# Kernel optimization log

Hardware: AMD Instinct MI355X
Metric: run time of the kernel (lower is better)

The kernel has to match this reference:

```python
import jax, jax.numpy as jnp
import numpy as np

B, P, K, HE, HF = 256, 128, 512, 1024, 512
D = K + HE + 2 * HF  # 2560, MLP input dim
HID = 64


def setup_inputs() -> dict:
    key = jax.random.key(0)
    ks = jax.random.split(key, 6)
    query = jax.random.normal(ks[0], (B, 1, HE), dtype=jnp.float32)
    keys = jax.random.normal(ks[1], (B, P, K), dtype=jnp.float32)
    frameLSTM_h = jax.random.normal(ks[2], (B, 1, 2 * HF), dtype=jnp.float32)
    mask = jax.random.randint(ks[3], (B, P), 0, 2, dtype=jnp.int32)
    mask = mask.at[:, 0].set(1)  # guarantee at least one unmasked player per row
    W1 = jax.random.normal(ks[4], (D, HID), dtype=jnp.float32) / np.float32(np.sqrt(D))
    W2 = jax.random.normal(ks[5], (HID, 1), dtype=jnp.float32) / np.float32(np.sqrt(HID))
    return dict(query=query, keys=keys, frameLSTM_h=frameLSTM_h, mask=mask, W1=W1, W2=W2)


def reference(query, keys, frameLSTM_h, mask, W1, W2):
    # Faithful to: cat([keys, query.repeat, frame.repeat]) @ W1 -> ReLU -> @ W2.
    # The pre-activation is linear, so splitting W1 by row-blocks is exactly the
    # same math without materializing the repeated/concatenated (B,P,D) tensor.
    W1k = W1[:K]            # (K, 64)
    W1q = W1[K:K + HE]      # (HE, 64)
    W1f = W1[K + HE:]       # (2*HF, 64)
    h = jax.nn.relu(
        jnp.einsum('bpk,kh->bph', keys, W1k)
        + jnp.einsum('boe,eh->boh', query, W1q)        # broadcasts over P
        + jnp.einsum('bof,fh->boh', frameLSTM_h, W1f)  # broadcasts over P
    )  # (B, P, 64)
    raw_scores = jnp.einsum('bph,ho->bp', h, W2)  # (B, P)
    raw_scores = jnp.where(mask == 0, -jnp.inf, raw_scores)
    weights = jax.nn.softmax(raw_scores, axis=1)  # (B, P)
    context = jnp.einsum('bp,bpk->bk', weights, keys)[:, None, :]  # (B, 1, K)
    embeddings = jnp.concatenate([context, frameLSTM_h], axis=2)   # (B, 1, K+2*HF)
    return embeddings, weights
```

## Files before the change

### kernel.cpp

```cpp
#include <hip/hip_runtime.h>
#include <hip/hip_bf16.h>
#include <cstdint>
#include <math.h>


typedef __bf16 bf16;
typedef __attribute__((ext_vector_type(8))) __bf16 bf16x8;
typedef __attribute__((ext_vector_type(4))) __bf16 bf16x4;
typedef __attribute__((ext_vector_type(4))) float f32x4;

#define NB 256
#define NP 128
#define NK 512
#define SKLD 520
#define SK_BYTES (NP * SKLD * 2)
#define SMEM_BYTES (SK_BYTES + 128*4 + 128*4 + 256*4 + 64*4)

__global__ __launch_bounds__(256) void prep_kernel(
    const float* __restrict__ W1, bf16* __restrict__ w1kt,
    bf16* __restrict__ w1qft)
{
    const int blk = blockIdx.x;
    const int t = threadIdx.x;
    __shared__ float s[32][65];
    if (blk < 16) {
        const int k0 = blk * 32;
#pragma unroll
        for (int i = 0; i < 8; i++) {
            const int idx = t + 256 * i;
            const int k = idx >> 6, h = idx & 63;
            s[k][h] = W1[(size_t)(k0 + k) * 64 + h];
        }
        __syncthreads();
#pragma unroll
        for (int i = 0; i < 8; i++) {
            const int idx = t + 256 * i;
            const int h = idx >> 5, kk = idx & 31;
            w1kt[(size_t)h * 512 + k0 + kk] = (bf16)s[kk][h];
        }
    } else {
        const int j = blk - 16;
        const int d0 = j * 32;
#pragma unroll
        for (int i = 0; i < 8; i++) {
            const int idx = t + 256 * i;
            const int r = idx >> 6, h = idx & 63;
            s[r][h] = W1[(size_t)(512 + d0 + r) * 64 + h];
        }
        __syncthreads();
#pragma unroll
        for (int i = 0; i < 8; i++) {
            const int idx = t + 256 * i;
            const int h = idx >> 5, rr = idx & 31;
            w1qft[(size_t)h * 2048 + d0 + rr] = (bf16)s[rr][h];
        }
    }
}

__global__ __launch_bounds__(256) void attn_kernel(
    const float* __restrict__ keys, const float* __restrict__ query,
    const float* __restrict__ frame, const int* __restrict__ mask,
    const float* __restrict__ W2, const bf16* __restrict__ w1kt,
    const bf16* __restrict__ w1qft, float* __restrict__ out)
{
    extern __shared__ char smem[];
    bf16* sk      = (bf16*)smem;
    float* scores = (float*)(smem + SK_BYTES);
    float* wts    = scores + 128;
    float* pp     = wts + 128;
    float* w2l    = pp + 256;

    const int b = blockIdx.x;
    const int t = threadIdx.x;
    const int w = t >> 6;
    const int lane = t & 63;
    const int m = lane & 15;
    const int q = lane >> 4;

    if (t < 64) w2l[t] = W2[t];

    {
        const float* qf = (w < 2 ? query : frame) + (size_t)b * 1024 + (w & 1) * 512;
        const bf16* wb = w1qft + (size_t)m * 2048 + w * 512 + q * 8;
        f32x4 pacc[4];
#pragma unroll
        for (int nt = 0; nt < 4; nt++) pacc[nt] = (f32x4){0.f, 0.f, 0.f, 0.f};

        float4 qa = *(const float4*)(qf + q * 8);
        float4 qb = *(const float4*)(qf + q * 8 + 4);
        bf16x8 Bp[4];
#pragma unroll
        for (int nt = 0; nt < 4; nt++) Bp[nt] = *(const bf16x8*)(wb + nt * 32768);

#pragma unroll
        for (int kk = 0; kk < 16; kk++) {
            bf16x8 Af;
            Af[0] = (bf16)qa.x; Af[1] = (bf16)qa.y; Af[2] = (bf16)qa.z; Af[3] = (bf16)qa.w;
            Af[4] = (bf16)qb.x; Af[5] = (bf16)qb.y; Af[6] = (bf16)qb.z; Af[7] = (bf16)qb.w;
            bf16x8 Bc[4];
#pragma unroll
            for (int nt = 0; nt < 4; nt++) Bc[nt] = Bp[nt];
            if (kk < 15) {
                qa = *(const float4*)(qf + (kk + 1) * 32 + q * 8);
                qb = *(const float4*)(qf + (kk + 1) * 32 + q * 8 + 4);
#pragma unroll
                for (int nt = 0; nt < 4; nt++)
                    Bp[nt] = *(const bf16x8*)(wb + nt * 32768 + (kk + 1) * 32);
            }
#pragma unroll
            for (int nt = 0; nt < 4; nt++)
                pacc[nt] = __builtin_amdgcn_mfma_f32_16x16x32_bf16(Af, Bc[nt], pacc[nt], 0, 0, 0);
        }
        if (q == 0) {
#pragma unroll
            for (int nt = 0; nt < 4; nt++)
                pp[w * 64 + nt * 16 + m] = pacc[nt][0];
        }
    }

    const float* kb = keys + (size_t)b * (NP * NK);
    {
        const int rowadd = t >> 7;
        const int c0 = (t & 127) * 4;
        float4 kv[2][16];
#pragma unroll
        for (int ii = 0; ii < 16; ii++)
            kv[0][ii] = *(const float4*)(kb + (size_t)ii * 1024 + t * 4);
#pragma unroll
        for (int jj = 0; jj < 4; jj++) {
            const int cur = jj & 1;
            if (jj < 3) {
#pragma unroll
                for (int ii = 0; ii < 16; ii++)
                    kv[cur ^ 1][ii] =
                        *(const float4*)(kb + (size_t)((jj + 1) * 16 + ii) * 1024 + t * 4);
            }
#pragma unroll
            for (int ii = 0; ii < 16; ii++) {
                const float4 v = kv[cur][ii];
                bf16x4 bv;
                bv[0] = (bf16)v.x; bv[1] = (bf16)v.y;
                bv[2] = (bf16)v.z; bv[3] = (bf16)v.w;
                *(bf16x4*)(sk + (size_t)(2 * (jj * 16 + ii) + rowadd) * SKLD + c0) = bv;
            }
        }
    }
    __syncthreads();

    const int pw = w * 32;
    const bf16* bbase = w1kt + (size_t)m * 512 + q * 8;

    bf16x8 Bv[2][16];
#pragma unroll
    for (int kk = 0; kk < 16; kk++)
        Bv[0][kk] = *(const bf16x8*)(bbase + kk * 32);

    float pr[2][4] = {{0.f,0.f,0.f,0.f},{0.f,0.f,0.f,0.f}};

#pragma unroll
    for (int nt = 0; nt < 4; nt++) {
        const int cur = nt & 1;
        if (nt < 3) {
#pragma unroll
            for (int kk = 0; kk < 16; kk++)
                Bv[cur ^ 1][kk] = *(const bf16x8*)(bbase + (nt + 1) * 8192 + kk * 32);
        }
        f32x4 acc0 = (f32x4){0.f,0.f,0.f,0.f};
        f32x4 acc1 = (f32x4){0.f,0.f,0.f,0.f};
#pragma unroll
        for (int kk = 0; kk < 16; kk++) {
            const int k0 = kk * 32 + q * 8;
            const bf16x8 A0 = *(const bf16x8*)(sk + (pw + m) * SKLD + k0);
            const bf16x8 A1 = *(const bf16x8*)(sk + (pw + 16 + m) * SKLD + k0);
            acc0 = __builtin_amdgcn_mfma_f32_16x16x32_bf16(A0, Bv[cur][kk], acc0, 0, 0, 0);
            acc1 = __builtin_amdgcn_mfma_f32_16x16x32_bf16(A1, Bv[cur][kk], acc1, 0, 0, 0);
        }
        const int h = nt * 16 + m;
        const float pv = pp[h] + pp[64 + h] + pp[128 + h] + pp[192 + h];
        const float wv = w2l[h];
#pragma unroll
        for (int r = 0; r < 4; r++) {
            pr[0][r] += fmaxf(acc0[r] + pv, 0.f) * wv;
            pr[1][r] += fmaxf(acc1[r] + pv, 0.f) * wv;
        }
    }

#pragma unroll
    for (int off = 1; off < 16; off <<= 1) {
#pragma unroll
        for (int mt = 0; mt < 2; mt++)
#pragma unroll
            for (int r = 0; r < 4; r++)
                pr[mt][r] += __shfl_xor(pr[mt][r], off);
    }
    if (m == 0) {
#pragma unroll
        for (int mt = 0; mt < 2; mt++) {
            const int pbase = pw + mt * 16 + q * 4;
#pragma unroll
            for (int r = 0; r < 4; r++) scores[pbase + r] = pr[mt][r];
        }
    }
    __syncthreads();

    if (w == 0) {
        const int pa = lane, pb = lane + 64;
        float s0 = (mask[b * 128 + pa] == 0) ? -INFINITY : scores[pa];
        float s1 = (mask[b * 128 + pb] == 0) ? -INFINITY : scores[pb];
        float mx = fmaxf(s0, s1);
#pragma unroll
        for (int off = 32; off; off >>= 1) mx = fmaxf(mx, __shfl_xor(mx, off));
        float e0 = __expf(s0 - mx), e1 = __expf(s1 - mx);
        float sum = e0 + e1;
#pragma unroll
        for (int off = 32; off; off >>= 1) sum += __shfl_xor(sum, off);
        const float inv = 1.0f / sum;
        e0 *= inv; e1 *= inv;
        wts[pa] = e0; wts[pb] = e1;
        float* wout = out + (size_t)NB * 1536;
        wout[b * 128 + pa] = e0;
        wout[b * 128 + pb] = e1;
    }
    __syncthreads();

    {
        float a0 = 0.f, a1 = 0.f;
        const int c = 2 * t;
#pragma unroll 8
        for (int p = 0; p < 128; p++) {
            const float wv = wts[p];
            const uint32_t uv = *(const uint32_t*)(sk + p * SKLD + c);
            a0 += wv * __uint_as_float(uv << 16);
            a1 += wv * __uint_as_float(uv & 0xffff0000u);
        }
        out[(size_t)b * 1536 + c] = a0;
        out[(size_t)b * 1536 + c + 1] = a1;
    }
    {
        const float4 fv = *(const float4*)(frame + (size_t)b * 1024 + t * 4);
        *(float4*)(out + (size_t)b * 1536 + 512 + t * 4) = fv;
    }
}

extern "C" void kernel_launch(void* const* d_in, const int* in_sizes, int n_in,
                              void* d_out, int out_size, void* d_ws, size_t ws_size,
                              hipStream_t stream) {
    const float* query = (const float*)d_in[0];
    const float* keys  = (const float*)d_in[1];
    const float* frame = (const float*)d_in[2];
    const int*   mask  = (const int*)d_in[3];
    const float* W1    = (const float*)d_in[4];
    const float* W2    = (const float*)d_in[5];
    float* out = (float*)d_out;

    bf16* w1kt  = (bf16*)d_ws;
    bf16* w1qft = (bf16*)((char*)d_ws + (64 << 10));

    hipFuncSetAttribute((const void*)attn_kernel,
                        hipFuncAttributeMaxDynamicSharedMemorySize, SMEM_BYTES);

    prep_kernel<<<80, 256, 0, stream>>>(W1, w1kt, w1qft);
    attn_kernel<<<256, 256, SMEM_BYTES, stream>>>(keys, query, frame, mask, W2,
                                                  w1kt, w1qft, out);
}
```

Baseline: 123.1 us.

## Double attention block to 512 threads and split work across eight waves

The attention kernel now launches 512 threads per batch row instead of 256. The query/frame projection is split across eight waves, with bf16 copies of the query and frame staged through shared memory. Each wave handles 16 players and keeps its A fragments in registers for the score MFMAs. The context reduction is split into two halves of players that are combined through shared memory. The goal is more in-flight memory traffic and latency hiding per block on a 256-block grid, at the cost of extra barriers, more shared memory and register pressure under launch_bounds(512,2).

New measurement: 129.7 us. 5.3% more time.

```diff
diff --git a/kernel.cpp b/kernel.cpp
--- a/kernel.cpp
+++ b/kernel.cpp
@@ -14,7 +14,13 @@
 #define NK 512
 #define SKLD 520
 #define SK_BYTES (NP * SKLD * 2)
-#define SMEM_BYTES (SK_BYTES + 128*4 + 128*4 + 256*4 + 64*4)
+#define SQF_OFF  SK_BYTES
+#define SCORES_OFF (SQF_OFF + 4096)
+#define WTS_OFF    (SCORES_OFF + 512)
+#define PP_OFF     (WTS_OFF + 512)
+#define W2_OFF     (PP_OFF + 2048)
+#define CP_OFF     (W2_OFF + 256)
+#define SMEM_BYTES (CP_OFF + 2048)
 
 __global__ __launch_bounds__(256) void prep_kernel(
     const float* __restrict__ W1, bf16* __restrict__ w1kt,
@@ -57,7 +63,7 @@
     }
 }
 
-__global__ __launch_bounds__(256) void attn_kernel(
+__global__ __launch_bounds__(512, 2) void attn_kernel(
     const float* __restrict__ keys, const float* __restrict__ query,
     const float* __restrict__ frame, const int* __restrict__ mask,
     const float* __restrict__ W2, const bf16* __restrict__ w1kt,
@@ -65,10 +71,12 @@
 {
     extern __shared__ char smem[];
     bf16* sk      = (bf16*)smem;
-    float* scores = (float*)(smem + SK_BYTES);
-    float* wts    = scores + 128;
-    float* pp     = wts + 128;
-    float* w2l    = pp + 256;
+    bf16* sqf     = (bf16*)(smem + SQF_OFF);
+    float* scores = (float*)(smem + SCORES_OFF);
+    float* wts    = (float*)(smem + WTS_OFF);
+    float* pp     = (float*)(smem + PP_OFF);
+    float* w2l    = (float*)(smem + W2_OFF);
+    float* cpart  = (float*)(smem + CP_OFF);
 
     const int b = blockIdx.x;
     const int t = threadIdx.x;
@@ -80,83 +88,88 @@
     if (t < 64) w2l[t] = W2[t];
 
     {
-        const float* qf = (w < 2 ? query : frame) + (size_t)b * 1024 + (w & 1) * 512;
-        const bf16* wb = w1qft + (size_t)m * 2048 + w * 512 + q * 8;
-        f32x4 pacc[4];
-#pragma unroll
-        for (int nt = 0; nt < 4; nt++) pacc[nt] = (f32x4){0.f, 0.f, 0.f, 0.f};
-
-        float4 qa = *(const float4*)(qf + q * 8);
-        float4 qb = *(const float4*)(qf + q * 8 + 4);
-        bf16x8 Bp[4];
-#pragma unroll
-        for (int nt = 0; nt < 4; nt++) Bp[nt] = *(const bf16x8*)(wb + nt * 32768);
-
-#pragma unroll
-        for (int kk = 0; kk < 16; kk++) {
-            bf16x8 Af;
-            Af[0] = (bf16)qa.x; Af[1] = (bf16)qa.y; Af[2] = (bf16)qa.z; Af[3] = (bf16)qa.w;
-            Af[4] = (bf16)qb.x; Af[5] = (bf16)qb.y; Af[6] = (bf16)qb.z; Af[7] = (bf16)qb.w;
-            bf16x8 Bc[4];
-#pragma unroll
-            for (int nt = 0; nt < 4; nt++) Bc[nt] = Bp[nt];
-            if (kk < 15) {
-                qa = *(const float4*)(qf + (kk + 1) * 32 + q * 8);
-                qb = *(const float4*)(qf + (kk + 1) * 32 + q * 8 + 4);
-#pragma unroll
-                for (int nt = 0; nt < 4; nt++)
-                    Bp[nt] = *(const bf16x8*)(wb + nt * 32768 + (kk + 1) * 32);
-            }
-#pragma unroll
-            for (int nt = 0; nt < 4; nt++)
-                pacc[nt] = __builtin_amdgcn_mfma_f32_16x16x32_bf16(Af, Bc[nt], pacc[nt], 0, 0, 0);
-        }
-        if (q == 0) {
-#pragma unroll
-            for (int nt = 0; nt < 4; nt++)
-                pp[w * 64 + nt * 16 + m] = pacc[nt][0];
-        }
-    }
-
-    const float* kb = keys + (size_t)b * (NP * NK);
-    {
+        const float* qsrc = (t < 256 ? query : frame) + (size_t)b * 1024 + (t & 255) * 4;
+        const float4 qv = *(const float4*)qsrc;
+
         const int rowadd = t >> 7;
         const int c0 = (t & 127) * 4;
-        float4 kv[2][16];
-#pragma unroll
-        for (int ii = 0; ii < 16; ii++)
-            kv[0][ii] = *(const float4*)(kb + (size_t)ii * 1024 + t * 4);
-#pragma unroll
-        for (int jj = 0; jj < 4; jj++) {
-            const int cur = jj & 1;
-            if (jj < 3) {
-#pragma unroll
-                for (int ii = 0; ii < 16; ii++)
-                    kv[cur ^ 1][ii] =
-                        *(const float4*)(kb + (size_t)((jj + 1) * 16 + ii) * 1024 + t * 4);
+        const float* kb = keys + (size_t)b * (NP * NK);
+        float4 kv[2][8];
+#pragma unroll
+        for (int ii = 0; ii < 8; ii++)
+            kv[0][ii] = *(const float4*)(kb + (size_t)(4 * ii + rowadd) * 512 + (t & 127) * 4);
+
+        bf16x4 qb;
+        qb[0] = (bf16)qv.x; qb[1] = (bf16)qv.y; qb[2] = (bf16)qv.z; qb[3] = (bf16)qv.w;
+        *(bf16x4*)(sqf + t * 4) = qb;
+
+#pragma unroll
+        for (int g = 0; g < 4; g++) {
+            const int cur = g & 1;
+            if (g < 3) {
+#pragma unroll
+                for (int ii = 0; ii < 8; ii++)
+                    kv[cur ^ 1][ii] = *(const float4*)(
+                        kb + (size_t)(4 * ((g + 1) * 8 + ii) + rowadd) * 512 + (t & 127) * 4);
             }
 #pragma unroll
-            for (int ii = 0; ii < 16; ii++) {
+            for (int ii = 0; ii < 8; ii++) {
                 const float4 v = kv[cur][ii];
                 bf16x4 bv;
                 bv[0] = (bf16)v.x; bv[1] = (bf16)v.y;
                 bv[2] = (bf16)v.z; bv[3] = (bf16)v.w;
-                *(bf16x4*)(sk + (size_t)(2 * (jj * 16 + ii) + rowadd) * SKLD + c0) = bv;
+                *(bf16x4*)(sk + (size_t)(4 * (g * 8 + ii) + rowadd) * SKLD + c0) = bv;
             }
         }
     }
     __syncthreads();
 
-    const int pw = w * 32;
+    {
+        const bf16* wb = w1qft + (size_t)m * 2048 + w * 256 + q * 8;
+        f32x4 pacc[4];
+#pragma unroll
+        for (int nt = 0; nt < 4; nt++) pacc[nt] = (f32x4){0.f, 0.f, 0.f, 0.f};
+
+        bf16x8 Bp[4];
+#pragma unroll
+        for (int nt = 0; nt < 4; nt++) Bp[nt] = *(const bf16x8*)(wb + nt * 32768);
+
+#pragma unroll
+        for (int kk = 0; kk < 8; kk++) {
+            const bf16x8 Af = *(const bf16x8*)(sqf + w * 256 + kk * 32 + q * 8);
+            bf16x8 Bc[4];
+#pragma unroll
+            for (int nt = 0; nt < 4; nt++) Bc[nt] = Bp[nt];
+            if (kk < 7) {
+#pragma unroll
+                for (int nt = 0; nt < 4; nt++)
+                    Bp[nt] = *(const bf16x8*)(wb + nt * 32768 + (kk + 1) * 32);
+            }
+#pragma unroll
+            for (int nt = 0; nt < 4; nt++)
+                pacc[nt] = __builtin_amdgcn_mfma_f32_16x16x32_bf16(Af, Bc[nt], pacc[nt], 0, 0, 0);
+        }
+        if (q == 0) {
+#pragma unroll
+            for (int nt = 0; nt < 4; nt++)
+                pp[w * 64 + nt * 16 + m] = pacc[nt][0];
+        }
+    }
+    __syncthreads();
+
+    const int pw = w * 16;
+    bf16x8 Av[16];
+#pragma unroll
+    for (int kk = 0; kk < 16; kk++)
+        Av[kk] = *(const bf16x8*)(sk + (pw + m) * SKLD + kk * 32 + q * 8);
+
     const bf16* bbase = w1kt + (size_t)m * 512 + q * 8;
-
     bf16x8 Bv[2][16];
 #pragma unroll
     for (int kk = 0; kk < 16; kk++)
         Bv[0][kk] = *(const bf16x8*)(bbase + kk * 32);
 
-    float pr[2][4] = {{0.f,0.f,0.f,0.f},{0.f,0.f,0.f,0.f}};
-
+    float pr[4] = {0.f, 0.f, 0.f, 0.f};
 #pragma unroll
     for (int nt = 0; nt < 4; nt++) {
         const int cur = nt & 1;
@@ -165,41 +178,28 @@
             for (int kk = 0; kk < 16; kk++)
                 Bv[cur ^ 1][kk] = *(const bf16x8*)(bbase + (nt + 1) * 8192 + kk * 32);
         }
-        f32x4 acc0 = (f32x4){0.f,0.f,0.f,0.f};
-        f32x4 acc1 = (f32x4){0.f,0.f,0.f,0.f};
-#pragma unroll
-        for (int kk = 0; kk < 16; kk++) {
-            const int k0 = kk * 32 + q * 8;
-            const bf16x8 A0 = *(const bf16x8*)(sk + (pw + m) * SKLD + k0);
-            const bf16x8 A1 = *(const bf16x8*)(sk + (pw + 16 + m) * SKLD + k0);
-            acc0 = __builtin_amdgcn_mfma_f32_16x16x32_bf16(A0, Bv[cur][kk], acc0, 0, 0, 0);
-            acc1 = __builtin_amdgcn_mfma_f32_16x16x32_bf16(A1, Bv[cur][kk], acc1, 0, 0, 0);
-        }
+        f32x4 acc = (f32x4){0.f, 0.f, 0.f, 0.f};
+#pragma unroll
+        for (int kk = 0; kk < 16; kk++)
+            acc = __builtin_amdgcn_mfma_f32_16x16x32_bf16(Av[kk], Bv[cur][kk], acc, 0, 0, 0);
         const int h = nt * 16 + m;
-        const float pv = pp[h] + pp[64 + h] + pp[128 + h] + pp[192 + h];
+        const float pv = pp[h] + pp[64 + h] + pp[128 + h] + pp[192 + h]
+                       + pp[256 + h] + pp[320 + h] + pp[384 + h] + pp[448 + h];
         const float wv = w2l[h];
 #pragma unroll
-        for (int r = 0; r < 4; r++) {
-            pr[0][r] += fmaxf(acc0[r] + pv, 0.f) * wv;
-            pr[1][r] += fmaxf(acc1[r] + pv, 0.f) * wv;
-        }
+        for (int r = 0; r < 4; r++)
+            pr[r] += fmaxf(acc[r] + pv, 0.f) * wv;
     }
 
 #pragma unroll
     for (int off = 1; off < 16; off <<= 1) {
 #pragma unroll
-        for (int mt = 0; mt < 2; mt++)
-#pragma unroll
-            for (int r = 0; r < 4; r++)
-                pr[mt][r] += __shfl_xor(pr[mt][r], off);
+        for (int r = 0; r < 4; r++) pr[r] += __shfl_xor(pr[r], off);
     }
     if (m == 0) {
-#pragma unroll
-        for (int mt = 0; mt < 2; mt++) {
-            const int pbase = pw + mt * 16 + q * 4;
-#pragma unroll
-            for (int r = 0; r < 4; r++) scores[pbase + r] = pr[mt][r];
-        }
+        const int pbase = pw + q * 4;
+#pragma unroll
+        for (int r = 0; r < 4; r++) scores[pbase + r] = pr[r];
     }
     __syncthreads();
 
@@ -224,21 +224,30 @@
     __syncthreads();
 
     {
+        const int tg = t >> 8;
+        const int tc = t & 255;
         float a0 = 0.f, a1 = 0.f;
-        const int c = 2 * t;
 #pragma unroll 8
-        for (int p = 0; p < 128; p++) {
+        for (int i = 0; i < 64; i++) {
+            const int p = tg * 64 + i;
             const float wv = wts[p];
-            const uint32_t uv = *(const uint32_t*)(sk + p * SKLD + c);
+            const uint32_t uv = *(const uint32_t*)(sk + (size_t)p * SKLD + 2 * tc);
             a0 += wv * __uint_as_float(uv << 16);
             a1 += wv * __uint_as_float(uv & 0xffff0000u);
         }
-        out[(size_t)b * 1536 + c] = a0;
-        out[(size_t)b * 1536 + c + 1] = a1;
-    }
-    {
-        const float4 fv = *(const float4*)(frame + (size_t)b * 1024 + t * 4);
-        *(float4*)(out + (size_t)b * 1536 + 512 + t * 4) = fv;
+        if (tg == 1) {
+            cpart[2 * tc] = a0;
+            cpart[2 * tc + 1] = a1;
+        }
+        __syncthreads();
+        if (tg == 0) {
+            out[(size_t)b * 1536 + 2 * tc]     = a0 + cpart[2 * tc];
+            out[(size_t)b * 1536 + 2 * tc + 1] = a1 + cpart[2 * tc + 1];
+        }
+    }
+    {
+        const float2 fv = *(const float2*)(frame + (size_t)b * 1024 + t * 2);
+        *(float2*)(out + (size_t)b * 1536 + 512 + t * 2) = fv;
     }
 }
 
@@ -260,6 +269,6 @@
                         hipFuncAttributeMaxDynamicSharedMemorySize, SMEM_BYTES);
 
     prep_kernel<<<80, 256, 0, stream>>>(W1, w1kt, w1qft);
-    attn_kernel<<<256, 256, SMEM_BYTES, stream>>>(keys, query, frame, mask, W2,
+    attn_kernel<<<256, 512, SMEM_BYTES, stream>>>(keys, query, frame, mask, W2,
                                                   w1kt, w1qft, out);
 }
```
